# Optimization experiments

Measured on AMD Instinct MI355X. Metric: run time of the kernel, lower is better.

## Reference

```python
import jax, jax.numpy as jnp
import numpy as np


def _scale_quantize(t, bits):
    # Mirrors scale_quantize(): affine quantization over global min/max.
    n = 2.0 ** bits - 1.0
    mn = t.min()
    mx = t.max()
    S = (mx - mn) / n
    Z = jnp.round(n * mn / (mn - mx))
    q = jnp.round((t - mn) / (mx - mn) * n)
    return q, S, Z


def setup_inputs() -> dict:
    key = jax.random.key(0)
    k1, k2, k3 = jax.random.split(key, 3)
    x = jax.random.normal(k1, (4, 2048, 4096), dtype=jnp.float32)
    W = jax.random.normal(k2, (4096, 4096), dtype=jnp.float32) * 0.02
    b = jax.random.normal(k3, (4096,), dtype=jnp.float32) * 0.01
    return {"x": x, "W": W, "b": b, "bits": 8}


def reference(x, W, b, bits):
    # Inference branch of ScaleQuant.forward (counter <= 0).
    n = 2.0 ** bits - 1.0
    # Weight quantization (done in __init__): q1, S1, Z1
    q1, S1, Z1 = _scale_quantize(W, bits)
    # Activation quant params (calibrated via scale_quantize on the input)
    _, S2, Z2 = _scale_quantize(x, bits)
    # input = clamp(round(x / S2 + Z2), 0, 2^bits - 1)
    xq = jnp.clip(jnp.round(x / S2 + Z2), 0.0, n)
    # quant_module.bias = round(bias / (S1 * S2))
    qb = jnp.round(b / (S1 * S2))
    # q1q2 = quant_module(input): xq @ q1^T + qb
    q1q2 = jnp.einsum('bsk,ok->bso', xq, q1) + qb
    # q1Z2 = m1(Z2 * ones): (Z2*ones) @ q1^T == Z2 * rowsum(q1) per out feature
    q1Z2 = Z2 * jnp.sum(q1, axis=1)                      # [d_out]
    # q2Z1 = m2(input): xq @ (Z1*ones)^T == Z1 * sum_k xq
    q2Z1 = Z1 * jnp.sum(xq, axis=-1, keepdims=True)      # [b, s, 1]
    # Z1Z2 = m3(ones): ones @ (Z1*Z2*ones)^T == Z1*Z2*d_in (scalar per element)
    Z1Z2 = Z1 * Z2 * W.shape[1]
    out = S1 * S2 * (q1q2 - (q1Z2 + q2Z1) + Z1Z2)
    return out
```

## Files before the change

kernel.cpp:

```cpp
#include <hip/hip_runtime.h>
#include <hip/hip_bf16.h>
#include <cstdint>
#include <math.h>

typedef int v4i __attribute__((ext_vector_type(4)));

__device__ __forceinline__ void atomicMinF(float* addr, float v) {
  if (v >= 0.f) atomicMin((int*)addr, __float_as_int(v));
  else          atomicMax((unsigned int*)addr, __float_as_uint(v));
}
__device__ __forceinline__ void atomicMaxF(float* addr, float v) {
  if (v >= 0.f) atomicMax((int*)addr, __float_as_int(v));
  else          atomicMin((unsigned int*)addr, __float_as_uint(v));
}

__global__ void init_params_kernel(float* p) {
  p[0] =  INFINITY;
  p[1] = -INFINITY;
  p[2] =  INFINITY;
  p[3] = -INFINITY;
}

__global__ __launch_bounds__(256) void minmax_kernel(const float* __restrict__ a, long long n,
                                                     float* mnp, float* mxp) {
  float mn = INFINITY, mx = -INFINITY;
  long long n4 = n >> 2;
  long long stride = (long long)gridDim.x * blockDim.x;
  for (long long i = (long long)blockIdx.x * blockDim.x + threadIdx.x; i < n4; i += stride) {
    float4 v = ((const float4*)a)[i];
    mn = fminf(mn, fminf(fminf(v.x, v.y), fminf(v.z, v.w)));
    mx = fmaxf(mx, fmaxf(fmaxf(v.x, v.y), fmaxf(v.z, v.w)));
  }
  if (blockIdx.x == 0 && threadIdx.x < (int)(n & 3)) {
    float v = a[n4 * 4 + threadIdx.x];
    mn = fminf(mn, v); mx = fmaxf(mx, v);
  }
  #pragma unroll
  for (int off = 32; off; off >>= 1) {
    mn = fminf(mn, __shfl_xor(mn, off));
    mx = fmaxf(mx, __shfl_xor(mx, off));
  }
  __shared__ float smn[4], smx[4];
  int wv = threadIdx.x >> 6;
  if ((threadIdx.x & 63) == 0) { smn[wv] = mn; smx[wv] = mx; }
  __syncthreads();
  if (threadIdx.x == 0) {
    mn = fminf(fminf(smn[0], smn[1]), fminf(smn[2], smn[3]));
    mx = fmaxf(fmaxf(smx[0], smx[1]), fmaxf(smx[2], smx[3]));
    atomicMinF(mnp, mn);
    atomicMaxF(mxp, mx);
  }
}

__global__ void compute_params_kernel(float* p, const int* bits, float Kf) {
  float n   = (float)((1u << bits[0]) - 1u);
  float xmn = p[0], xmx = p[1], wmn = p[2], wmx = p[3];
  float S1 = (wmx - wmn) / n;
  float Z1 = rintf(n * wmn / (wmn - wmx));
  float S2 = (xmx - xmn) / n;
  float Z2 = rintf(n * xmn / (xmn - xmx));
  float s1s2 = S1 * S2;
  p[4]  = s1s2;
  p[5]  = 128.0f - Z2;
  p[6]  = 128.0f - Z1;
  p[7]  = (Z1 * Z2 - 16384.0f) * Kf;
  p[8]  = S2;
  p[9]  = Z2;
  p[10] = wmn;
  p[11] = wmx - wmn;
  p[12] = n;
}

__global__ __launch_bounds__(256) void quant_w_kernel(const float* __restrict__ W,
                                                      const float* __restrict__ bias,
                                                      const float* __restrict__ p,
                                                      int8_t* __restrict__ q1,
                                                      float* __restrict__ colC, int K) {
  const int o = blockIdx.x;
  const float wmn = p[10], wrng = p[11], n = p[12], s1s2 = p[4], cW = p[5], cC = p[7];
  const float4* Wr = (const float4*)(W + (size_t)o * K);
  unsigned int* qr = (unsigned int*)(q1 + (size_t)o * K);
  int sum = 0;
  const int K4 = K >> 2;
  for (int c = threadIdx.x; c < K4; c += 256) {
    float4 v = Wr[c];
    int q0 = (int)rintf((v.x - wmn) / wrng * n);
    int q1i = (int)rintf((v.y - wmn) / wrng * n);
    int q2 = (int)rintf((v.z - wmn) / wrng * n);
    int q3 = (int)rintf((v.w - wmn) / wrng * n);
    sum += q0 + q1i + q2 + q3;
    qr[c] = ((unsigned)((q0 - 128) & 255))
          | ((unsigned)((q1i - 128) & 255) << 8)
          | ((unsigned)((q2 - 128) & 255) << 16)
          | ((unsigned)((q3 - 128) & 255) << 24);
  }
  #pragma unroll
  for (int off = 32; off; off >>= 1) sum += __shfl_xor(sum, off);
  __shared__ int ps[4];
  if ((threadIdx.x & 63) == 0) ps[threadIdx.x >> 6] = sum;
  __syncthreads();
  if (threadIdx.x == 0) {
    float tot = (float)(ps[0] + ps[1] + ps[2] + ps[3]);
    colC[o] = cW * tot + rintf(bias[o] / s1s2) + cC;
  }
}

__global__ __launch_bounds__(256) void quant_x_kernel(const float* __restrict__ x,
                                                      const float* __restrict__ p,
                                                      int8_t* __restrict__ xq,
                                                      float* __restrict__ rowC, int K) {
  const int i = blockIdx.x;
  const float S2 = p[8], Z2 = p[9], n = p[12], cX = p[6];
  const float4* xr = (const float4*)(x + (size_t)i * K);
  unsigned int* qr = (unsigned int*)(xq + (size_t)i * K);
  int sum = 0;
  const int K4 = K >> 2;
  for (int c = threadIdx.x; c < K4; c += 256) {
    float4 v = xr[c];
    int q0 = (int)fminf(fmaxf(rintf(v.x / S2 + Z2), 0.f), n);
    int q1i = (int)fminf(fmaxf(rintf(v.y / S2 + Z2), 0.f), n);
    int q2 = (int)fminf(fmaxf(rintf(v.z / S2 + Z2), 0.f), n);
    int q3 = (int)fminf(fmaxf(rintf(v.w / S2 + Z2), 0.f), n);
    sum += q0 + q1i + q2 + q3;
    qr[c] = ((unsigned)((q0 - 128) & 255))
          | ((unsigned)((q1i - 128) & 255) << 8)
          | ((unsigned)((q2 - 128) & 255) << 16)
          | ((unsigned)((q3 - 128) & 255) << 24);
  }
  #pragma unroll
  for (int off = 32; off; off >>= 1) sum += __shfl_xor(sum, off);
  __shared__ int ps[4];
  if ((threadIdx.x & 63) == 0) ps[threadIdx.x >> 6] = sum;
  __syncthreads();
  if (threadIdx.x == 0) {
    float tot = (float)(ps[0] + ps[1] + ps[2] + ps[3]);
    rowC[i] = cX * tot;
  }
}

__device__ __forceinline__ void gload_lds16(const void* g, void* l) {
  __builtin_amdgcn_global_load_lds((const __attribute__((address_space(1))) void*)g,
                                   (__attribute__((address_space(3))) void*)l, 16, 0, 0);
}

__global__ __launch_bounds__(256) void gemm_i8_kernel(const int8_t* __restrict__ xq,
                                                      const int8_t* __restrict__ q1,
                                                      const float* __restrict__ p,
                                                      const float* __restrict__ colC,
                                                      const float* __restrict__ rowC,
                                                      float* __restrict__ out,
                                                      int M, int N, int K) {
  __shared__ int8_t As[128 * 64];
  __shared__ int8_t Bs[128 * 64];

  const int tid  = threadIdx.x;
  const int lane = tid & 63;
  const int wv   = tid >> 6;
  const int wr   = wv >> 1;
  const int wc   = wv & 1;
  const int bm   = blockIdx.y;
  const int bn   = blockIdx.x;
  const int r15  = lane & 15;
  const int kg   = lane >> 4;

  v4i acc[4][4];
  #pragma unroll
  for (int m = 0; m < 4; ++m)
    #pragma unroll
    for (int n = 0; n < 4; ++n) { v4i z = {0, 0, 0, 0}; acc[m][n] = z; }

  const size_t Abase = (size_t)bm * 128 * K;
  const size_t Bbase = (size_t)bn * 128 * K;
  const int srow = tid >> 2;
  const int sseg = tid & 3;
  const int sw = ((kg ^ (r15 & 3)) << 4);

  for (int kt = 0; kt < K; kt += 64) {
    __syncthreads();
    #pragma unroll
    for (int i = 0; i < 2; ++i) {
      int row = i * 64 + srow;
      int sg  = sseg ^ (row & 3);
      gload_lds16(xq + Abase + (size_t)row * K + kt + sg * 16,
                  &As[i * 4096 + wv * 1024 + lane * 16]);
      gload_lds16(q1 + Bbase + (size_t)row * K + kt + sg * 16,
                  &Bs[i * 4096 + wv * 1024 + lane * 16]);
    }
    __syncthreads();

    v4i af[4], bf[4];
    #pragma unroll
    for (int m = 0; m < 4; ++m)
      af[m] = *(const v4i*)&As[(wr * 64 + m * 16 + r15) * 64 + sw];
    #pragma unroll
    for (int n = 0; n < 4; ++n)
      bf[n] = *(const v4i*)&Bs[(wc * 64 + n * 16 + r15) * 64 + sw];
    #pragma unroll
    for (int m = 0; m < 4; ++m)
      #pragma unroll
      for (int n = 0; n < 4; ++n)
        acc[m][n] = __builtin_amdgcn_mfma_i32_16x16x64_i8(af[m], bf[n], acc[m][n], 0, 0, 0);
  }

  const float s1s2 = p[4];
  const int orow0 = bm * 128 + wr * 64;
  const int ocol0 = bn * 128 + wc * 64;
  #pragma unroll
  for (int n = 0; n < 4; ++n) {
    const int go = ocol0 + n * 16 + r15;
    const float cc = colC[go];
    #pragma unroll
    for (int m = 0; m < 4; ++m) {
      const int gibase = orow0 + m * 16 + kg * 4;
      #pragma unroll
      for (int r = 0; r < 4; ++r) {
        const int gi = gibase + r;
        out[(size_t)gi * N + go] = s1s2 * ((float)acc[m][n][r] + cc + rowC[gi]);
      }
    }
  }
}

extern "C" void kernel_launch(void* const* d_in, const int* in_sizes, int n_in,
                              void* d_out, int out_size, void* d_ws, size_t ws_size,
                              hipStream_t stream) {
  const float* x    = (const float*)d_in[0];
  const float* W    = (const float*)d_in[1];
  const float* b    = (const float*)d_in[2];
  const int*   bits = (const int*)d_in[3];

  const long long xN = in_sizes[0];
  const long long wN = in_sizes[1];
  const int O = in_sizes[2];
  const int K = (int)(wN / O);
  const int M = (int)(xN / K);

  char* ws = (char*)d_ws;
  float* p    = (float*)ws;
  float* colC = (float*)(ws + 256);
  size_t off = 256 + (size_t)O * sizeof(float);
  off = (off + 255) & ~(size_t)255;
  float* rowC = (float*)(ws + off);
  off += (size_t)M * sizeof(float);
  off = (off + 255) & ~(size_t)255;
  int8_t* q1 = (int8_t*)(ws + off);
  off += (size_t)O * (size_t)K;
  int8_t* xq = (int8_t*)(ws + off);

  init_params_kernel<<<1, 1, 0, stream>>>(p);
  minmax_kernel<<<512, 256, 0, stream>>>(x, xN, p + 0, p + 1);
  minmax_kernel<<<512, 256, 0, stream>>>(W, wN, p + 2, p + 3);
  compute_params_kernel<<<1, 1, 0, stream>>>(p, bits, (float)K);
  quant_w_kernel<<<O, 256, 0, stream>>>(W, b, p, q1, colC, K);
  quant_x_kernel<<<M, 256, 0, stream>>>(x, p, xq, rowC, K);

  dim3 grid(O / 128, M / 128);
  gemm_i8_kernel<<<grid, 256, 0, stream>>>(xq, q1, p, colC, rowC, (float*)d_out, M, O, K);
}
```

Before: 556.3 us.

## Double-buffer GEMM LDS loads, remap workgroups, and unroll minmax/quant loops

The int8 GEMM now uses two LDS buffers, so the next K-tile's global-to-LDS loads are issued before the current tile's MFMAs run. This removes one barrier per iteration. Workgroups move to a 1D grid with an XCD-aware index remap, and the LDS swizzle pattern changes. Separately, the minmax and quantize kernels are unrolled 4x with independent accumulators, and the minmax grid grows to 2048 blocks. Risks: doubled LDS use lowers occupancy, and the new swizzle must stay consistent between writers and readers.

```diff
diff --git a/kernel.cpp b/kernel.cpp
--- a/kernel.cpp
+++ b/kernel.cpp
@@ -23,18 +23,35 @@
 
 __global__ __launch_bounds__(256) void minmax_kernel(const float* __restrict__ a, long long n,
                                                      float* mnp, float* mxp) {
-  float mn = INFINITY, mx = -INFINITY;
-  long long n4 = n >> 2;
-  long long stride = (long long)gridDim.x * blockDim.x;
-  for (long long i = (long long)blockIdx.x * blockDim.x + threadIdx.x; i < n4; i += stride) {
-    float4 v = ((const float4*)a)[i];
-    mn = fminf(mn, fminf(fminf(v.x, v.y), fminf(v.z, v.w)));
-    mx = fmaxf(mx, fmaxf(fmaxf(v.x, v.y), fmaxf(v.z, v.w)));
-  }
+  const float4* a4 = (const float4*)a;
+  const long long n4 = n >> 2;
+  const long long tid = (long long)blockIdx.x * blockDim.x + threadIdx.x;
+  const long long stride = (long long)gridDim.x * blockDim.x * 4;
+  float mn0 = INFINITY, mx0 = -INFINITY, mn1 = INFINITY, mx1 = -INFINITY;
+  float mn2 = INFINITY, mx2 = -INFINITY, mn3 = INFINITY, mx3 = -INFINITY;
   if (blockIdx.x == 0 && threadIdx.x < (int)(n & 3)) {
     float v = a[n4 * 4 + threadIdx.x];
-    mn = fminf(mn, v); mx = fmaxf(mx, v);
-  }
+    mn0 = fminf(mn0, v); mx0 = fmaxf(mx0, v);
+  }
+  long long i = tid * 4;
+  for (; i + 4 <= n4; i += stride) {
+    float4 v0 = a4[i], v1 = a4[i + 1], v2 = a4[i + 2], v3 = a4[i + 3];
+    mn0 = fminf(mn0, fminf(fminf(v0.x, v0.y), fminf(v0.z, v0.w)));
+    mx0 = fmaxf(mx0, fmaxf(fmaxf(v0.x, v0.y), fmaxf(v0.z, v0.w)));
+    mn1 = fminf(mn1, fminf(fminf(v1.x, v1.y), fminf(v1.z, v1.w)));
+    mx1 = fmaxf(mx1, fmaxf(fmaxf(v1.x, v1.y), fmaxf(v1.z, v1.w)));
+    mn2 = fminf(mn2, fminf(fminf(v2.x, v2.y), fminf(v2.z, v2.w)));
+    mx2 = fmaxf(mx2, fmaxf(fmaxf(v2.x, v2.y), fmaxf(v2.z, v2.w)));
+    mn3 = fminf(mn3, fminf(fminf(v3.x, v3.y), fminf(v3.z, v3.w)));
+    mx3 = fmaxf(mx3, fmaxf(fmaxf(v3.x, v3.y), fmaxf(v3.z, v3.w)));
+  }
+  for (; i < n4; ++i) {
+    float4 v = a4[i];
+    mn0 = fminf(mn0, fminf(fminf(v.x, v.y), fminf(v.z, v.w)));
+    mx0 = fmaxf(mx0, fmaxf(fmaxf(v.x, v.y), fmaxf(v.z, v.w)));
+  }
+  float mn = fminf(fminf(mn0, mn1), fminf(mn2, mn3));
+  float mx = fmaxf(fmaxf(mx0, mx1), fmaxf(mx2, mx3));
   #pragma unroll
   for (int off = 32; off; off >>= 1) {
     mn = fminf(mn, __shfl_xor(mn, off));
@@ -71,6 +88,25 @@
   p[12] = n;
 }
 
+__device__ __forceinline__ unsigned qpack_w(float4 v, float wmn, float wrng, float n, int& sum) {
+  int q0 = (int)rintf((v.x - wmn) / wrng * n);
+  int q1 = (int)rintf((v.y - wmn) / wrng * n);
+  int q2 = (int)rintf((v.z - wmn) / wrng * n);
+  int q3 = (int)rintf((v.w - wmn) / wrng * n);
+  sum += q0 + q1 + q2 + q3;
+  return ((unsigned)((q0 - 128) & 255)) | ((unsigned)((q1 - 128) & 255) << 8)
+       | ((unsigned)((q2 - 128) & 255) << 16) | ((unsigned)((q3 - 128) & 255) << 24);
+}
+__device__ __forceinline__ unsigned qpack_x(float4 v, float S2, float Z2, float n, int& sum) {
+  int q0 = (int)fminf(fmaxf(rintf(v.x / S2 + Z2), 0.f), n);
+  int q1 = (int)fminf(fmaxf(rintf(v.y / S2 + Z2), 0.f), n);
+  int q2 = (int)fminf(fmaxf(rintf(v.z / S2 + Z2), 0.f), n);
+  int q3 = (int)fminf(fmaxf(rintf(v.w / S2 + Z2), 0.f), n);
+  sum += q0 + q1 + q2 + q3;
+  return ((unsigned)((q0 - 128) & 255)) | ((unsigned)((q1 - 128) & 255) << 8)
+       | ((unsigned)((q2 - 128) & 255) << 16) | ((unsigned)((q3 - 128) & 255) << 24);
+}
+
 __global__ __launch_bounds__(256) void quant_w_kernel(const float* __restrict__ W,
                                                       const float* __restrict__ bias,
                                                       const float* __restrict__ p,
@@ -82,18 +118,15 @@
   unsigned int* qr = (unsigned int*)(q1 + (size_t)o * K);
   int sum = 0;
   const int K4 = K >> 2;
-  for (int c = threadIdx.x; c < K4; c += 256) {
-    float4 v = Wr[c];
-    int q0 = (int)rintf((v.x - wmn) / wrng * n);
-    int q1i = (int)rintf((v.y - wmn) / wrng * n);
-    int q2 = (int)rintf((v.z - wmn) / wrng * n);
-    int q3 = (int)rintf((v.w - wmn) / wrng * n);
-    sum += q0 + q1i + q2 + q3;
-    qr[c] = ((unsigned)((q0 - 128) & 255))
-          | ((unsigned)((q1i - 128) & 255) << 8)
-          | ((unsigned)((q2 - 128) & 255) << 16)
-          | ((unsigned)((q3 - 128) & 255) << 24);
-  }
+  int c = threadIdx.x;
+  for (; c + 768 < K4; c += 1024) {
+    float4 v0 = Wr[c], v1 = Wr[c + 256], v2 = Wr[c + 512], v3 = Wr[c + 768];
+    qr[c]       = qpack_w(v0, wmn, wrng, n, sum);
+    qr[c + 256] = qpack_w(v1, wmn, wrng, n, sum);
+    qr[c + 512] = qpack_w(v2, wmn, wrng, n, sum);
+    qr[c + 768] = qpack_w(v3, wmn, wrng, n, sum);
+  }
+  for (; c < K4; c += 256) qr[c] = qpack_w(Wr[c], wmn, wrng, n, sum);
   #pragma unroll
   for (int off = 32; off; off >>= 1) sum += __shfl_xor(sum, off);
   __shared__ int ps[4];
@@ -115,18 +148,15 @@
   unsigned int* qr = (unsigned int*)(xq + (size_t)i * K);
   int sum = 0;
   const int K4 = K >> 2;
-  for (int c = threadIdx.x; c < K4; c += 256) {
-    float4 v = xr[c];
-    int q0 = (int)fminf(fmaxf(rintf(v.x / S2 + Z2), 0.f), n);
-    int q1i = (int)fminf(fmaxf(rintf(v.y / S2 + Z2), 0.f), n);
-    int q2 = (int)fminf(fmaxf(rintf(v.z / S2 + Z2), 0.f), n);
-    int q3 = (int)fminf(fmaxf(rintf(v.w / S2 + Z2), 0.f), n);
-    sum += q0 + q1i + q2 + q3;
-    qr[c] = ((unsigned)((q0 - 128) & 255))
-          | ((unsigned)((q1i - 128) & 255) << 8)
-          | ((unsigned)((q2 - 128) & 255) << 16)
-          | ((unsigned)((q3 - 128) & 255) << 24);
-  }
+  int c = threadIdx.x;
+  for (; c + 768 < K4; c += 1024) {
+    float4 v0 = xr[c], v1 = xr[c + 256], v2 = xr[c + 512], v3 = xr[c + 768];
+    qr[c]       = qpack_x(v0, S2, Z2, n, sum);
+    qr[c + 256] = qpack_x(v1, S2, Z2, n, sum);
+    qr[c + 512] = qpack_x(v2, S2, Z2, n, sum);
+    qr[c + 768] = qpack_x(v3, S2, Z2, n, sum);
+  }
+  for (; c < K4; c += 256) qr[c] = qpack_x(xr[c], S2, Z2, n, sum);
   #pragma unroll
   for (int off = 32; off; off >>= 1) sum += __shfl_xor(sum, off);
   __shared__ int ps[4];
@@ -150,18 +180,27 @@
                                                       const float* __restrict__ rowC,
                                                       float* __restrict__ out,
                                                       int M, int N, int K) {
-  __shared__ int8_t As[128 * 64];
-  __shared__ int8_t Bs[128 * 64];
+  __shared__ int8_t As[2][128 * 64];
+  __shared__ int8_t Bs[2][128 * 64];
 
   const int tid  = threadIdx.x;
   const int lane = tid & 63;
   const int wv   = tid >> 6;
   const int wr   = wv >> 1;
   const int wc   = wv & 1;
-  const int bm   = blockIdx.y;
-  const int bn   = blockIdx.x;
   const int r15  = lane & 15;
   const int kg   = lane >> 4;
+
+  const int nwg = gridDim.x;
+  const int nbn = N >> 7;
+  int tl;
+  if ((nwg & 7) == 0) {
+    tl = (blockIdx.x & 7) * (nwg >> 3) + (blockIdx.x >> 3);
+  } else {
+    tl = blockIdx.x;
+  }
+  const int bm = tl / nbn;
+  const int bn = tl % nbn;
 
   v4i acc[4][4];
   #pragma unroll
@@ -173,33 +212,45 @@
   const size_t Bbase = (size_t)bn * 128 * K;
   const int srow = tid >> 2;
   const int sseg = tid & 3;
-  const int sw = ((kg ^ (r15 & 3)) << 4);
-
-  for (int kt = 0; kt < K; kt += 64) {
-    __syncthreads();
-    #pragma unroll
-    for (int i = 0; i < 2; ++i) {
-      int row = i * 64 + srow;
-      int sg  = sseg ^ (row & 3);
-      gload_lds16(xq + Abase + (size_t)row * K + kt + sg * 16,
-                  &As[i * 4096 + wv * 1024 + lane * 16]);
-      gload_lds16(q1 + Bbase + (size_t)row * K + kt + sg * 16,
-                  &Bs[i * 4096 + wv * 1024 + lane * 16]);
+  const int sg   = sseg ^ ((srow >> 2) & 3);
+  const int swoff = ((kg ^ ((r15 >> 2) & 3)) << 4);
+
+  const int NT = K >> 6;
+
+  #pragma unroll
+  for (int i = 0; i < 2; ++i) {
+    const size_t roff = (size_t)(i * 64 + srow) * K + sg * 16;
+    gload_lds16(xq + Abase + roff, &As[0][i * 4096 + tid * 16]);
+    gload_lds16(q1 + Bbase + roff, &Bs[0][i * 4096 + tid * 16]);
+  }
+  __syncthreads();
+
+  for (int kt = 0; kt < NT; ++kt) {
+    const int cur = kt & 1;
+    if (kt + 1 < NT) {
+      const int kof = (kt + 1) << 6;
+      #pragma unroll
+      for (int i = 0; i < 2; ++i) {
+        const size_t roff = (size_t)(i * 64 + srow) * K + kof + sg * 16;
+        gload_lds16(xq + Abase + roff, &As[cur ^ 1][i * 4096 + tid * 16]);
+        gload_lds16(q1 + Bbase + roff, &Bs[cur ^ 1][i * 4096 + tid * 16]);
+      }
     }
-    __syncthreads();
-
+    const int8_t* as = As[cur];
+    const int8_t* bs = Bs[cur];
     v4i af[4], bf[4];
     #pragma unroll
     for (int m = 0; m < 4; ++m)
-      af[m] = *(const v4i*)&As[(wr * 64 + m * 16 + r15) * 64 + sw];
+      af[m] = *(const v4i*)&as[(wr * 64 + m * 16 + r15) * 64 + swoff];
     #pragma unroll
     for (int n = 0; n < 4; ++n)
-      bf[n] = *(const v4i*)&Bs[(wc * 64 + n * 16 + r15) * 64 + sw];
+      bf[n] = *(const v4i*)&bs[(wc * 64 + n * 16 + r15) * 64 + swoff];
     #pragma unroll
     for (int m = 0; m < 4; ++m)
       #pragma unroll
       for (int n = 0; n < 4; ++n)
         acc[m][n] = __builtin_amdgcn_mfma_i32_16x16x64_i8(af[m], bf[n], acc[m][n], 0, 0, 0);
+    __syncthreads();
   }
 
   const float s1s2 = p[4];
@@ -248,12 +299,12 @@
   int8_t* xq = (int8_t*)(ws + off);
 
   init_params_kernel<<<1, 1, 0, stream>>>(p);
-  minmax_kernel<<<512, 256, 0, stream>>>(x, xN, p + 0, p + 1);
-  minmax_kernel<<<512, 256, 0, stream>>>(W, wN, p + 2, p + 3);
+  minmax_kernel<<<2048, 256, 0, stream>>>(x, xN, p + 0, p + 1);
+  minmax_kernel<<<2048, 256, 0, stream>>>(W, wN, p + 2, p + 3);
   compute_params_kernel<<<1, 1, 0, stream>>>(p, bits, (float)K);
   quant_w_kernel<<<O, 256, 0, stream>>>(W, b, p, q1, colC, K);
   quant_x_kernel<<<M, 256, 0, stream>>>(x, p, xq, rowC, K);
 
-  dim3 grid(O / 128, M / 128);
-  gemm_i8_kernel<<<grid, 256, 0, stream>>>(xq, q1, p, colC, rowC, (float*)d_out, M, O, K);
-}
+  const int nwg = (M / 128) * (O / 128);
+  gemm_i8_kernel<<<nwg, 256, 0, stream>>>(xq, q1, p, colC, rowC, (float*)d_out, M, O, K);
+}
```

New measurement: 574.1 us. 1.03x slower.
